# Kernel optimization log

Hardware: AMD Instinct MI355X
Metric: run time of the kernel (lower is better)

Reference implementation:

```python
import jax, jax.numpy as jnp
import numpy as np

# TT-linear: in_features=1024 -> out_features=4096
IN_DIMS = (8, 8, 4, 4)      # m1..m4, prod = 1024
OUT_DIMS = (8, 8, 8, 8)     # n1..n4, prod = 4096
RANKS = (1, 16, 16, 16, 1)  # r0..r4
IN_FEATURES = 1024
OUT_FEATURES = 4096
BATCH, SEQ = 4, 1024


def _init_core(key, shape):
    # uniform(-1,1)/sqrt(fan_in-ish), matching the original's uniform-style init scale
    fan = shape[0] * shape[1]
    return (2.0 * jax.random.uniform(key, shape, dtype=jnp.float32) - 1.0) / np.sqrt(fan).astype(np.float32)


def setup_inputs() -> dict:
    key = jax.random.key(0)
    ks = jax.random.split(key, 6)
    x = jax.random.normal(ks[0], (BATCH, SEQ, IN_FEATURES), dtype=jnp.float32)
    core0 = _init_core(ks[1], (1, 8, 8, 16))    # [r0, m1, n1, r1]
    core1 = _init_core(ks[2], (16, 8, 8, 16))   # [r1, m2, n2, r2]
    core2 = _init_core(ks[3], (16, 4, 8, 16))   # [r2, m3, n3, r3]
    core3 = _init_core(ks[4], (16, 4, 8, 1))    # [r3, m4, n4, r4]
    bias = (2.0 * jax.random.uniform(ks[5], (OUT_FEATURES,), dtype=jnp.float32) - 1.0) / np.sqrt(OUT_FEATURES).astype(np.float32)
    return {"x": x, "core0": core0, "core1": core1, "core2": core2, "core3": core3, "bias": bias}


def reference(x, core0, core1, core2, core3, bias):
    lead = x.shape[:-1]
    # split the feature axis into TT input factors: [T, m1, m2, m3, m4]
    t = x.reshape((-1,) + IN_DIMS)
    c0 = core0[0]        # [m1, n1, r1]   (boundary rank r0 = 1 squeezed)
    c3 = core3[..., 0]   # [r3, m4, n4]   (boundary rank r4 = 1 squeezed)
    # sequential TT core chain: absorb one m_k, emit one n_k per step
    t = jnp.einsum('tijkl,ixp->tjklxp', t, c0)      # [T, m2,m3,m4, n1, r1]
    t = jnp.einsum('tjklxp,pjyq->tklxyq', t, core1)  # [T, m3,m4, n1,n2, r2]
    t = jnp.einsum('tklxyq,qkzr->tlxyzr', t, core2)  # [T, m4, n1,n2,n3, r3]
    t = jnp.einsum('tlxyzr,rlw->txyzw', t, c3)       # [T, n1,n2,n3,n4]
    y = t.reshape(lead + (OUT_FEATURES,)) + bias
    return y
```

## Files before the change

kernel.cpp:

```cpp
#include <hip/hip_runtime.h>
#include <hip/hip_bf16.h>
#include <cstdint>


typedef __bf16 bf16x8 __attribute__((ext_vector_type(8)));
typedef float f32x4 __attribute__((ext_vector_type(4)));

__device__ __forceinline__ void g2lds16(const void* g, void* l) {
    __builtin_amdgcn_global_load_lds(
        (const __attribute__((address_space(1))) void*)g,
        (__attribute__((address_space(3))) void*)l,
        16, 0, 0);
}

__global__ __launch_bounds__(256) void prep(
    const float* __restrict__ x, __bf16* __restrict__ xb,
    const float* __restrict__ c0, const float* __restrict__ c1,
    const float* __restrict__ c2, const float* __restrict__ c3,
    __bf16* __restrict__ wt) {
    const int b = blockIdx.x;
    const int t = threadIdx.x;
    if (b < 2048) {
        const int i = (b * 256 + t) * 8;
        float4 a0 = *(const float4*)(x + i);
        float4 a1 = *(const float4*)(x + i + 4);
        bf16x8 o;
        o[0] = (__bf16)a0.x; o[1] = (__bf16)a0.y; o[2] = (__bf16)a0.z; o[3] = (__bf16)a0.w;
        o[4] = (__bf16)a1.x; o[5] = (__bf16)a1.y; o[6] = (__bf16)a1.z; o[7] = (__bf16)a1.w;
        *(bf16x8*)(xb + i) = o;
        return;
    }
    __shared__ float t12[4][16];
    __shared__ float t123[4][512];
    __shared__ float c3s[512];
    #pragma unroll
    for (int i = t; i < 512; i += 256) c3s[i] = c3[i];
    const int s = t >> 6;
    const int lane = t & 63;
    const int g = (b - 2048) * 4 + s;
    const int m1 = g >> 9, n1 = (g >> 6) & 7, m2 = (g >> 3) & 7, n2 = g & 7;
    __syncthreads();
    if (lane < 16) {
        const int r2 = lane;
        float sum = 0.f;
        #pragma unroll
        for (int r1 = 0; r1 < 16; ++r1)
            sum += c0[(m1 * 8 + n1) * 16 + r1] * c1[((r1 * 8 + m2) * 8 + n2) * 16 + r2];
        t12[s][r2] = sum;
    }
    __syncthreads();
    #pragma unroll
    for (int idx = lane; idx < 512; idx += 64) {
        const int m3 = idx >> 7, n3 = (idx >> 4) & 7, r3 = idx & 15;
        float sum = 0.f;
        #pragma unroll
        for (int r2 = 0; r2 < 16; ++r2)
            sum += t12[s][r2] * c2[((r2 * 4 + m3) * 8 + n3) * 16 + r3];
        t123[s][(m3 * 8 + n3) * 16 + r3] = sum;
    }
    __syncthreads();
    const int n3 = lane >> 3, n4 = lane & 7;
    const int n = ((n1 * 8 + n2) * 8 + n3) * 8 + n4;
    const int kbase = (m1 * 8 + m2) * 16;
    float v[16];
    #pragma unroll
    for (int e = 0; e < 16; ++e) v[e] = 0.f;
    #pragma unroll
    for (int m3 = 0; m3 < 4; ++m3) {
        #pragma unroll
        for (int r3 = 0; r3 < 16; ++r3) {
            const float tv = t123[s][(m3 * 8 + n3) * 16 + r3];
            #pragma unroll
            for (int m4 = 0; m4 < 4; ++m4)
                v[m3 * 4 + m4] += tv * c3s[(r3 * 4 + m4) * 8 + n4];
        }
    }
    bf16x8 lo, hi;
    #pragma unroll
    for (int e = 0; e < 8; ++e) { lo[e] = (__bf16)v[e]; hi[e] = (__bf16)v[8 + e]; }
    *(bf16x8*)(wt + (size_t)n * 1024 + kbase)     = lo;
    *(bf16x8*)(wt + (size_t)n * 1024 + kbase + 8) = hi;
}


#define SCHED() __builtin_amdgcn_sched_barrier(0)
#define BAR()  do { SCHED(); __builtin_amdgcn_s_barrier(); SCHED(); } while (0)
#define WAITVM(n) do { SCHED(); asm volatile("s_waitcnt vmcnt(" #n ")"); SCHED(); } while (0)

__global__ __launch_bounds__(512, 4) void tt_gemm(
    const __bf16* __restrict__ A, const __bf16* __restrict__ B,
    const float* __restrict__ bias, float* __restrict__ C) {
    constexpr int K = 1024, N = 4096;
    constexpr int NKT = 32;
    __shared__ __bf16 sA[3][256 * 32];
    __shared__ __bf16 sB[3][128 * 32];
    const int t = threadIdx.x;
    const int lane = t & 63;
    const int wave = t >> 6;
    const int wm = (wave >> 2) * 128;
    const int wn = (wave & 3) * 32;
    const int l15 = lane & 15, lh = lane >> 4;
    const int cOff = ((lh ^ ((l15 >> 1) & 3)) << 4);

    const int xcd = blockIdx.x & 7;
    const int lid = blockIdx.x >> 3;
    const int bmo = ((xcd >> 2) * 8 + (lid & 7)) * 256;
    const int bno = ((xcd & 3) * 8 + (lid >> 3)) * 128;

    const int c0i = t, c1i = t + 512;
    const int rA0 = c0i >> 2, rA1 = c1i >> 2;
    const int lcA0 = (c0i & 3) ^ ((rA0 >> 1) & 3);
    const int lcA1 = (c1i & 3) ^ ((rA1 >> 1) & 3);
    const int rB = t >> 2;
    const int lcB = (t & 3) ^ ((rB >> 1) & 3);
    const __bf16* a0p = A + (size_t)(bmo + rA0) * K + lcA0 * 8;
    const __bf16* a1p = A + (size_t)(bmo + rA1) * K + lcA1 * 8;
    const __bf16* bp  = B + (size_t)(bno + rB)  * K + lcB * 8;

#define ST_A(kt, sl) do { \
    g2lds16(a0p + (size_t)(kt) * 32, (char*)&sA[sl][0] + c0i * 16); \
    g2lds16(a1p + (size_t)(kt) * 32, (char*)&sA[sl][0] + c1i * 16); } while (0)
#define ST_B(kt, sl) \
    g2lds16(bp + (size_t)(kt) * 32, (char*)&sB[sl][0] + t * 16)
#define LDA(dst, fi) dst = *(const bf16x8*)((const char*)&sA[s0][0] + (wm + (fi) * 16 + l15) * 64 + cOff)
#define LDB(dst, ni) dst = *(const bf16x8*)((const char*)&sB[s0][0] + (wn + (ni) * 16 + l15) * 64 + cOff)
#define MFMA8(base, afr) do { \
    __builtin_amdgcn_s_setprio(1); \
    _Pragma("unroll") \
    for (int mi = 0; mi < 4; ++mi) \
        _Pragma("unroll") \
        for (int ni = 0; ni < 2; ++ni) \
            acc[(base) + mi][ni] = __builtin_amdgcn_mfma_f32_16x16x32_bf16( \
                afr[mi], bb[ni], acc[(base) + mi][ni], 0, 0, 0); \
    __builtin_amdgcn_s_setprio(0); } while (0)

    f32x4 acc[8][2] = {};

    ST_A(0, 0); ST_B(0, 0);
    ST_A(1, 1); ST_B(1, 1);
    WAITVM(3);
    BAR();

    #pragma unroll 1
    for (int kt = 0; kt < NKT; ++kt) {
        const int s0 = kt % 3;
        const int s2 = (kt + 2) % 3;
        bf16x8 aL[4], aH[4], bb[2];
        #pragma unroll
        for (int mi = 0; mi < 4; ++mi) LDA(aL[mi], mi);
        #pragma unroll
        for (int ni = 0; ni < 2; ++ni) LDB(bb[ni], ni);
        if (kt < NKT - 2) ST_A(kt + 2, s2);
        BAR();
        MFMA8(0, aL);
        BAR();
        #pragma unroll
        for (int mi = 0; mi < 4; ++mi) LDA(aH[mi], 4 + mi);
        if (kt < NKT - 2) ST_B(kt + 2, s2);
        BAR();
        MFMA8(4, aH);
        if (kt < NKT - 2)       { WAITVM(3); }
        else if (kt == NKT - 2) { WAITVM(0); }
        BAR();
    }

    float bv[2];
    #pragma unroll
    for (int ni = 0; ni < 2; ++ni) bv[ni] = bias[bno + wn + ni * 16 + l15];
    #pragma unroll
    for (int mi = 0; mi < 8; ++mi) {
        #pragma unroll
        for (int r = 0; r < 4; ++r) {
            const int row = bmo + wm + mi * 16 + lh * 4 + r;
            float* crow = C + (size_t)row * N + bno + wn + l15;
            crow[0]  = acc[mi][0][r] + bv[0];
            crow[16] = acc[mi][1][r] + bv[1];
        }
    }
#undef ST_A
#undef ST_B
#undef LDA
#undef LDB
#undef MFMA8
}

extern "C" void kernel_launch(void* const* d_in, const int* in_sizes, int n_in,
                              void* d_out, int out_size, void* d_ws, size_t ws_size,
                              hipStream_t stream) {
    const float* x    = (const float*)d_in[0];
    const float* c0   = (const float*)d_in[1];
    const float* c1   = (const float*)d_in[2];
    const float* c2   = (const float*)d_in[3];
    const float* c3   = (const float*)d_in[4];
    const float* bias = (const float*)d_in[5];
    float* out = (float*)d_out;

    __bf16* xb = (__bf16*)d_ws;
    __bf16* wt = xb + (size_t)4096 * 1024;

    prep<<<3072, 256, 0, stream>>>(x, xb, c0, c1, c2, c3, wt);
    tt_gemm<<<512, 512, 0, stream>>>(xb, wt, bias, out);
}
```

Baseline: 137.4 us.

## Reshape per-wave tile to 64x64 and issue all loads before one MFMA phase

Each wave's output tile changes from 128x32 to 64x64, with 4x4 accumulators instead of 8x2. A and B fragments are now loaded together per k-step, which cuts LDS reads per wave (8 fragments instead of 10). The split two-phase MFMA schedule with extra barriers is collapsed into a single phase with one barrier per iteration. The intent is fewer barriers and better LDS reuse, at the cost of less interleaving between LDS reads, async global-to-LDS issue and MFMA work.

Result: no change. 136.5 us (median of 2 runs) (-0.6%).

```diff
diff --git a/kernel.cpp b/kernel.cpp
--- a/kernel.cpp
+++ b/kernel.cpp
@@ -97,15 +97,15 @@
     const int t = threadIdx.x;
     const int lane = t & 63;
     const int wave = t >> 6;
-    const int wm = (wave >> 2) * 128;
-    const int wn = (wave & 3) * 32;
+    const int wm = (wave >> 1) * 64;
+    const int wn = (wave & 1) * 64;
     const int l15 = lane & 15, lh = lane >> 4;
     const int cOff = ((lh ^ ((l15 >> 1) & 3)) << 4);
 
     const int xcd = blockIdx.x & 7;
     const int lid = blockIdx.x >> 3;
-    const int bmo = ((xcd >> 2) * 8 + (lid & 7)) * 256;
-    const int bno = ((xcd & 3) * 8 + (lid >> 3)) * 128;
+    const int bm = ((xcd >> 2) * 8 + (lid & 7)) * 256;
+    const int bn = ((xcd & 3) * 8 + (lid >> 3)) * 128;
 
     const int c0i = t, c1i = t + 512;
     const int rA0 = c0i >> 2, rA1 = c1i >> 2;
@@ -113,31 +113,21 @@
     const int lcA1 = (c1i & 3) ^ ((rA1 >> 1) & 3);
     const int rB = t >> 2;
     const int lcB = (t & 3) ^ ((rB >> 1) & 3);
-    const __bf16* a0p = A + (size_t)(bmo + rA0) * K + lcA0 * 8;
-    const __bf16* a1p = A + (size_t)(bmo + rA1) * K + lcA1 * 8;
-    const __bf16* bp  = B + (size_t)(bno + rB)  * K + lcB * 8;
+    const __bf16* a0p = A + (size_t)(bm + rA0) * K + lcA0 * 8;
+    const __bf16* a1p = A + (size_t)(bm + rA1) * K + lcA1 * 8;
+    const __bf16* bp  = B + (size_t)(bn + rB)  * K + lcB * 8;
 
-#define ST_A(kt, sl) do { \
+#define ST(kt, sl) do { \
     g2lds16(a0p + (size_t)(kt) * 32, (char*)&sA[sl][0] + c0i * 16); \
-    g2lds16(a1p + (size_t)(kt) * 32, (char*)&sA[sl][0] + c1i * 16); } while (0)
-#define ST_B(kt, sl) \
-    g2lds16(bp + (size_t)(kt) * 32, (char*)&sB[sl][0] + t * 16)
-#define LDA(dst, fi) dst = *(const bf16x8*)((const char*)&sA[s0][0] + (wm + (fi) * 16 + l15) * 64 + cOff)
+    g2lds16(a1p + (size_t)(kt) * 32, (char*)&sA[sl][0] + c1i * 16); \
+    g2lds16(bp  + (size_t)(kt) * 32, (char*)&sB[sl][0] + t * 16); } while (0)
+#define LDA(dst, mi) dst = *(const bf16x8*)((const char*)&sA[s0][0] + (wm + (mi) * 16 + l15) * 64 + cOff)
 #define LDB(dst, ni) dst = *(const bf16x8*)((const char*)&sB[s0][0] + (wn + (ni) * 16 + l15) * 64 + cOff)
-#define MFMA8(base, afr) do { \
-    __builtin_amdgcn_s_setprio(1); \
-    _Pragma("unroll") \
-    for (int mi = 0; mi < 4; ++mi) \
-        _Pragma("unroll") \
-        for (int ni = 0; ni < 2; ++ni) \
-            acc[(base) + mi][ni] = __builtin_amdgcn_mfma_f32_16x16x32_bf16( \
-                afr[mi], bb[ni], acc[(base) + mi][ni], 0, 0, 0); \
-    __builtin_amdgcn_s_setprio(0); } while (0)
 
-    f32x4 acc[8][2] = {};
+    f32x4 acc[4][4] = {};
 
-    ST_A(0, 0); ST_B(0, 0);
-    ST_A(1, 1); ST_B(1, 1);
+    ST(0, 0);
+    ST(1, 1);
     WAITVM(3);
     BAR();
 
@@ -145,43 +135,42 @@
     for (int kt = 0; kt < NKT; ++kt) {
         const int s0 = kt % 3;
         const int s2 = (kt + 2) % 3;
-        bf16x8 aL[4], aH[4], bb[2];
+        bf16x8 af[4], bf[4];
         #pragma unroll
-        for (int mi = 0; mi < 4; ++mi) LDA(aL[mi], mi);
+        for (int mi = 0; mi < 4; ++mi) LDA(af[mi], mi);
         #pragma unroll
-        for (int ni = 0; ni < 2; ++ni) LDB(bb[ni], ni);
-        if (kt < NKT - 2) ST_A(kt + 2, s2);
-        BAR();
-        MFMA8(0, aL);
-        BAR();
+        for (int ni = 0; ni < 4; ++ni) LDB(bf[ni], ni);
+        if (kt < NKT - 2) ST(kt + 2, s2);
+        __builtin_amdgcn_s_setprio(1);
         #pragma unroll
-        for (int mi = 0; mi < 4; ++mi) LDA(aH[mi], 4 + mi);
-        if (kt < NKT - 2) ST_B(kt + 2, s2);
-        BAR();
-        MFMA8(4, aH);
+        for (int mi = 0; mi < 4; ++mi)
+            #pragma unroll
+            for (int ni = 0; ni < 4; ++ni)
+                acc[mi][ni] = __builtin_amdgcn_mfma_f32_16x16x32_bf16(
+                    af[mi], bf[ni], acc[mi][ni], 0, 0, 0);
+        __builtin_amdgcn_s_setprio(0);
         if (kt < NKT - 2)       { WAITVM(3); }
         else if (kt == NKT - 2) { WAITVM(0); }
         BAR();
     }
 
-    float bv[2];
+    float bv[4];
     #pragma unroll
-    for (int ni = 0; ni < 2; ++ni) bv[ni] = bias[bno + wn + ni * 16 + l15];
+    for (int ni = 0; ni < 4; ++ni) bv[ni] = bias[bn + wn + ni * 16 + l15];
     #pragma unroll
-    for (int mi = 0; mi < 8; ++mi) {
+    for (int mi = 0; mi < 4; ++mi) {
         #pragma unroll
         for (int r = 0; r < 4; ++r) {
-            const int row = bmo + wm + mi * 16 + lh * 4 + r;
-            float* crow = C + (size_t)row * N + bno + wn + l15;
-            crow[0]  = acc[mi][0][r] + bv[0];
-            crow[16] = acc[mi][1][r] + bv[1];
+            const int row = bm + wm + mi * 16 + lh * 4 + r;
+            float* crow = C + (size_t)row * N + bn + wn + l15;
+            #pragma unroll
+            for (int ni = 0; ni < 4; ++ni)
+                crow[ni * 16] = acc[mi][ni][r] + bv[ni];
         }
     }
-#undef ST_A
-#undef ST_B
+#undef ST
 #undef LDA
 #undef LDB
-#undef MFMA8
 }
 
 extern "C" void kernel_launch(void* const* d_in, const int* in_sizes, int n_in,
```
